# Kernel optimization log

Hardware: AMD Instinct MI355X
Metric: run time of the kernel (lower is better)

## Reference

```python
import jax, jax.numpy as jnp
import numpy as np

SEQ_LEN = 4096
N_FEATURES = 2048
N_HIDDEN = 2048
TAGS = 10
START_TAG = 8
STOP_TAG = 9
H = N_HIDDEN // 2  # per-direction hidden size


def setup_inputs() -> dict:
    key = jax.random.key(0)
    ks = jax.random.split(key, 10)
    s = 0.02
    sentence = jax.random.normal(ks[0], (SEQ_LEN, 1, N_FEATURES), jnp.float32)
    W_ih_f = jax.random.normal(ks[1], (4 * H, N_FEATURES), jnp.float32) * s
    W_hh_f = jax.random.normal(ks[2], (4 * H, H), jnp.float32) * s
    b_f = jax.random.normal(ks[3], (4 * H,), jnp.float32) * s
    W_ih_b = jax.random.normal(ks[4], (4 * H, N_FEATURES), jnp.float32) * s
    W_hh_b = jax.random.normal(ks[5], (4 * H, H), jnp.float32) * s
    b_b = jax.random.normal(ks[6], (4 * H,), jnp.float32) * s
    W_lin = jax.random.normal(ks[7], (TAGS, N_HIDDEN), jnp.float32) * s
    b_lin = jax.random.normal(ks[8], (TAGS,), jnp.float32) * s
    transitions = jax.random.normal(ks[9], (TAGS, TAGS), jnp.float32)
    transitions = transitions.at[START_TAG, :].set(-10000.0).at[:, STOP_TAG].set(-10000.0)
    return {"sentence": sentence, "W_ih_f": W_ih_f, "W_hh_f": W_hh_f, "b_f": b_f,
            "W_ih_b": W_ih_b, "W_hh_b": W_hh_b, "b_b": b_b,
            "W_lin": W_lin, "b_lin": b_lin, "transitions": transitions}


def _lstm_dir(x, W_ih, W_hh, b, reverse):
    # Precompute the input projection for all timesteps (one big GEMM).
    xp = jnp.einsum('tbf,gf->tbg', x, W_ih) + b  # [T, B, 4H]
    B = x.shape[1]
    init = (jnp.zeros((B, H), x.dtype), jnp.zeros((B, H), x.dtype))

    def step(carry, g):
        h, c = carry
        gates = g + h @ W_hh.T  # [B, 4H], PyTorch gate order i, f, g, o
        i, f, gg, o = jnp.split(gates, 4, axis=-1)
        c = jax.nn.sigmoid(f) * c + jax.nn.sigmoid(i) * jnp.tanh(gg)
        h = jax.nn.sigmoid(o) * jnp.tanh(c)
        return (h, c), h

    _, hs = jax.lax.scan(step, init, xp, reverse=reverse)
    return hs  # [T, B, H]


def reference(sentence, W_ih_f, W_hh_f, b_f, W_ih_b, W_hh_b, b_b, W_lin, b_lin, transitions):
    h_f = _lstm_dir(sentence, W_ih_f, W_hh_f, b_f, False)
    h_b = _lstm_dir(sentence, W_ih_b, W_hh_b, b_b, True)
    lstm_out = jnp.concatenate([h_f, h_b], axis=-1)         # [T, 1, N_HIDDEN]
    feats = lstm_out @ W_lin.T + b_lin                       # [T, 1, TAGS]
    f = feats[:, 0, :]                                       # [T, TAGS] (batch=1 as in original)

    init_v = jnp.full((TAGS,), -10000.0, f.dtype).at[START_TAG].set(0.0)

    def vstep(fv, feat):
        scores = fv[None, :] + transitions                   # [next_tag, prev_tag]
        return jnp.max(scores, axis=1) + feat, jnp.argmax(scores, axis=1)

    fv, bps = jax.lax.scan(vstep, init_v, f)                 # bps: [T, TAGS]
    terminal = fv + transitions[STOP_TAG]
    path_score = jnp.max(terminal)
    best_last = jnp.argmax(terminal)

    def bstep(tag, bp):
        return bp[tag], tag

    _, best_path = jax.lax.scan(bstep, best_last, bps, reverse=True)  # [T] in time order
    return path_score, best_path
```

## Files before the change

kernel.cpp:

```cpp
#include <hip/hip_runtime.h>

typedef _Float16 f16;
typedef _Float16 f16x4 __attribute__((ext_vector_type(4)));
typedef _Float16 f16x8 __attribute__((ext_vector_type(8)));
typedef float f32x4 __attribute__((ext_vector_type(4)));
typedef unsigned u32x4 __attribute__((ext_vector_type(4)));

#define SEQ 4096
#define NF  2048
#define HID 1024
#define SENT 0x7F800001u

__device__ f16   g_Ahi[SEQ * NF];
__device__ f16   g_Alo[SEQ * NF];
__device__ f16   g_Whi[2 * 4096 * NF];
__device__ f16   g_Wlo[2 * 4096 * NF];
__device__ float g_xp [2u * SEQ * 4096u];
__device__ float g_hist[2u * SEQ * HID];
__device__ float g_ring[2][8][1024];
__device__ float g_feats[SEQ * 10];

__global__ void cvt_split(const float* __restrict__ src, int which, int n4) {
  int i = blockIdx.x * blockDim.x + threadIdx.x;
  int stride = gridDim.x * blockDim.x;
  f16* hi; f16* lo;
  if (which == 0)      { hi = g_Ahi; lo = g_Alo; }
  else if (which == 1) { hi = g_Whi; lo = g_Wlo; }
  else                 { hi = g_Whi + 4096 * NF; lo = g_Wlo + 4096 * NF; }
  const float4* s4 = (const float4*)src;
  f16x4* h4 = (f16x4*)hi;
  f16x4* l4 = (f16x4*)lo;
  for (int idx = i; idx < n4; idx += stride) {
    float4 v = s4[idx];
    f16x4 h, l;
    h.x = (f16)v.x; l.x = (f16)(v.x - (float)h.x);
    h.y = (f16)v.y; l.y = (f16)(v.y - (float)h.y);
    h.z = (f16)v.z; l.z = (f16)(v.z - (float)h.z);
    h.w = (f16)v.w; l.w = (f16)(v.w - (float)h.w);
    h4[idx] = h; l4[idx] = l;
  }
}

__global__ __launch_bounds__(256, 1) void gemm_xp(
    const float* __restrict__ b_f, const float* __restrict__ b_b)
{
  const int d = blockIdx.z;
  const f16* WhiD = g_Whi + (size_t)d * (4096u * 2048u);
  const f16* WloD = g_Wlo + (size_t)d * (4096u * 2048u);
  const float* bias = d ? b_b : b_f;
  float* out = g_xp + (size_t)d * (4096u * 4096u);

  __shared__ f16 sAh[128 * 40];
  __shared__ f16 sAl[128 * 40];
  __shared__ f16 sWh[128 * 40];
  __shared__ f16 sWl[128 * 40];

  const int tid  = threadIdx.x;
  const int lane = tid & 63;
  const int wv   = tid >> 6;
  const int quad = lane >> 4;
  const int mrow = lane & 15;
  const int m0 = (wv & 1) * 64;
  const int n0 = (wv >> 1) * 64;
  const int bm = blockIdx.y, bn = blockIdx.x;

  f32x4 acc[4][4] = {};

  const int r0  = tid >> 2;
  const int seg = tid & 3;

  for (int kt = 0; kt < 2048; kt += 32) {
#pragma unroll
    for (int r = 0; r < 2; ++r) {
      int row = r * 64 + r0;
      size_t ga = (size_t)(bm * 128 + row) * 2048 + kt + seg * 8;
      size_t gw = (size_t)(bn * 128 + row) * 2048 + kt + seg * 8;
      int lidx = row * 40 + seg * 8;
      *(f16x8*)&sAh[lidx] = *(const f16x8*)&g_Ahi[ga];
      *(f16x8*)&sAl[lidx] = *(const f16x8*)&g_Alo[ga];
      *(f16x8*)&sWh[lidx] = *(const f16x8*)&WhiD[gw];
      *(f16x8*)&sWl[lidx] = *(const f16x8*)&WloD[gw];
    }
    __syncthreads();

    f16x8 ah[4], al[4], wh[4], wl[4];
#pragma unroll
    for (int mi = 0; mi < 4; ++mi) {
      int rowm = (m0 + mi * 16 + mrow) * 40 + quad * 8;
      ah[mi] = *(const f16x8*)&sAh[rowm];
      al[mi] = *(const f16x8*)&sAl[rowm];
    }
#pragma unroll
    for (int ni = 0; ni < 4; ++ni) {
      int rown = (n0 + ni * 16 + mrow) * 40 + quad * 8;
      wh[ni] = *(const f16x8*)&sWh[rown];
      wl[ni] = *(const f16x8*)&sWl[rown];
    }
#pragma unroll
    for (int mi = 0; mi < 4; ++mi)
#pragma unroll
      for (int ni = 0; ni < 4; ++ni) {
        acc[mi][ni] = __builtin_amdgcn_mfma_f32_16x16x32_f16(ah[mi], wh[ni], acc[mi][ni], 0, 0, 0);
        acc[mi][ni] = __builtin_amdgcn_mfma_f32_16x16x32_f16(ah[mi], wl[ni], acc[mi][ni], 0, 0, 0);
        acc[mi][ni] = __builtin_amdgcn_mfma_f32_16x16x32_f16(al[mi], wh[ni], acc[mi][ni], 0, 0, 0);
      }
    __syncthreads();
  }

#pragma unroll
  for (int ni = 0; ni < 4; ++ni) {
    int g = bn * 128 + n0 + ni * 16 + mrow;
    float bv = bias[g];
#pragma unroll
    for (int mi = 0; mi < 4; ++mi) {
#pragma unroll
      for (int r = 0; r < 4; ++r) {
        int t = bm * 128 + m0 + mi * 16 + quad * 4 + r;
        out[(size_t)t * 4096 + g] = acc[mi][ni][r] + bv;
      }
    }
  }
}

__global__ void init_sync() {
  int i = blockIdx.x * blockDim.x + threadIdx.x;
  int slot = (i >> 10) & 7;
  ((unsigned*)g_ring)[i] = (slot == 0) ? 0u : SENT;
}

__global__ __launch_bounds__(1024) void lstm_persistent(
    const float* __restrict__ Whh_f, const float* __restrict__ Whh_b)
{
  const int bid = blockIdx.x;
  const int dir = bid & 3;
  if (dir >= 2) return;
  const int wsl = bid >> 2;
  const int tid = threadIdx.x;
  const int r   = tid >> 4;
  const int l16 = tid & 15;

  __shared__ float h_lds[1024];
  __shared__ float gates_lds[64];

  const float* Wd = dir ? Whh_b : Whh_f;

  const int grow = (r >> 4) * 1024 + wsl * 16 + (r & 15);
  float4 w4[16];
#pragma unroll
  for (int j = 0; j < 16; ++j)
    w4[j] = *(const float4*)&Wd[(size_t)grow * 1024 + 4 * l16 + 64 * j];

  const float* xpd = g_xp + (size_t)dir * 4096u * 4096u;
  float* histd = g_hist + (size_t)dir * 4096u * 1024u;
  float* ringd = &g_ring[dir][0][0];

  float c = 0.f;

  for (int t = 1; t <= 4096; ++t) {
    const int tau = dir ? (4096 - t) : (t - 1);

    float xv0 = 0.f, xv1 = 0.f, xv2 = 0.f, xv3 = 0.f;
    if (tid < 16) {
      const float* px = xpd + (size_t)tau * 4096 + wsl * 16 + tid;
      xv0 = px[0]; xv1 = px[1024]; xv2 = px[2048]; xv3 = px[3072];
    }

    if (tid < 256) {
      const float* rs = ringd + (size_t)((t - 1) & 7) * 1024 + 4 * tid;
      u32x4 q;
      for (;;) {
        asm volatile("global_load_dwordx4 %0, %1, off sc0 sc1\n\t"
                     "s_waitcnt vmcnt(0)"
                     : "=v"(q) : "v"(rs) : "memory");
        if (q.x != SENT && q.y != SENT && q.z != SENT && q.w != SENT) break;
        __builtin_amdgcn_s_sleep(1);
      }
      float4 hv;
      hv.x = __uint_as_float(q.x);
      hv.y = __uint_as_float(q.y);
      hv.z = __uint_as_float(q.z);
      hv.w = __uint_as_float(q.w);
      *(float4*)&h_lds[4 * tid] = hv;
    }
    __syncthreads();

    float p0 = 0.f, p1 = 0.f, p2 = 0.f, p3 = 0.f;
#pragma unroll
    for (int j = 0; j < 16; j += 4) {
      float4 h0 = *(const float4*)&h_lds[4 * l16 + 64 * (j + 0)];
      float4 h1 = *(const float4*)&h_lds[4 * l16 + 64 * (j + 1)];
      float4 h2 = *(const float4*)&h_lds[4 * l16 + 64 * (j + 2)];
      float4 h3 = *(const float4*)&h_lds[4 * l16 + 64 * (j + 3)];
      p0 += w4[j+0].x*h0.x + w4[j+0].y*h0.y + w4[j+0].z*h0.z + w4[j+0].w*h0.w;
      p1 += w4[j+1].x*h1.x + w4[j+1].y*h1.y + w4[j+1].z*h1.z + w4[j+1].w*h1.w;
      p2 += w4[j+2].x*h2.x + w4[j+2].y*h2.y + w4[j+2].z*h2.z + w4[j+2].w*h2.w;
      p3 += w4[j+3].x*h3.x + w4[j+3].y*h3.y + w4[j+3].z*h3.z + w4[j+3].w*h3.w;
    }
    float acc = (p0 + p1) + (p2 + p3);
    acc += __shfl_xor(acc, 1);
    acc += __shfl_xor(acc, 2);
    acc += __shfl_xor(acc, 4);
    acc += __shfl_xor(acc, 8);
    if (l16 == 0) gates_lds[r] = acc;
    __syncthreads();

    if (tid < 16) {
      float gi = gates_lds[tid]      + xv0;
      float gf = gates_lds[16 + tid] + xv1;
      float gg = gates_lds[32 + tid] + xv2;
      float go = gates_lds[48 + tid] + xv3;
      float si = 1.f / (1.f + __expf(-gi));
      float sf = 1.f / (1.f + __expf(-gf));
      float so = 1.f / (1.f + __expf(-go));
      float tg = 1.f - 2.f / (1.f + __expf(2.f * gg));
      c = sf * c + si * tg;
      float th = 1.f - 2.f / (1.f + __expf(2.f * c));
      float h  = so * th;
      const int dim = wsl * 16 + tid;
      __hip_atomic_store((unsigned*)&ringd[(size_t)(t & 7) * 1024 + dim],
                         __float_as_uint(h),
                         __ATOMIC_RELAXED, __HIP_MEMORY_SCOPE_AGENT);
      if (t + 4 <= 4096)
        __hip_atomic_store((unsigned*)&ringd[(size_t)((t + 4) & 7) * 1024 + dim],
                           SENT,
                           __ATOMIC_RELAXED, __HIP_MEMORY_SCOPE_AGENT);
      histd[(size_t)tau * 1024 + dim] = h;
    }
  }
}

__global__ __launch_bounds__(256, 1) void feats_kernel(
    const float* __restrict__ W_lin, const float* __restrict__ b_lin)
{
  const int tid = threadIdx.x;
  const int wv = tid >> 6, l = tid & 63;
  const int t0 = blockIdx.x * 16 + wv * 4;
  for (int it = 0; it < 4; ++it) {
    const int t = t0 + it;
    float hf[16], hbv[16];
#pragma unroll
    for (int i = 0; i < 16; ++i) hf[i]  = g_hist[(size_t)t * 1024 + l + 64 * i];
#pragma unroll
    for (int i = 0; i < 16; ++i) hbv[i] = g_hist[(size_t)(4096 + t) * 1024 + l + 64 * i];
#pragma unroll
    for (int tag = 0; tag < 10; ++tag) {
      float a = 0.f;
#pragma unroll
      for (int i = 0; i < 16; ++i) {
        a += W_lin[tag * 2048 + l + 64 * i] * hf[i];
        a += W_lin[tag * 2048 + 1024 + l + 64 * i] * hbv[i];
      }
      a += __shfl_xor(a, 32); a += __shfl_xor(a, 16); a += __shfl_xor(a, 8);
      a += __shfl_xor(a, 4);  a += __shfl_xor(a, 2);  a += __shfl_xor(a, 1);
      if (l == 0) g_feats[t * 10 + tag] = a + b_lin[tag];
    }
  }
}

__global__ __launch_bounds__(64, 1) void viterbi_kernel(
    const float* __restrict__ trans, float* __restrict__ out)
{
  __shared__ unsigned char bps[4096 * 10];
  const int to = threadIdx.x;
  float tr[10];
#pragma unroll
  for (int f = 0; f < 10; ++f) tr[f] = (to < 10) ? trans[to * 10 + f] : 0.f;
  float fv = (to == 8) ? 0.f : -10000.f;

  float fbuf[8];
#pragma unroll
  for (int i = 0; i < 8; ++i) fbuf[i] = (to < 10) ? g_feats[i * 10 + to] : 0.f;

  for (int t = 0; t < 4096; t += 8) {
#pragma unroll
    for (int u = 0; u < 8; ++u) {
      const int tt = t + u;
      float m = -3.4e38f; int am = 0;
#pragma unroll
      for (int f = 0; f < 10; ++f) {
        float v = __shfl(fv, f) + tr[f];
        if (v > m) { m = v; am = f; }
      }
      float ft = fbuf[u];
      if (tt + 8 < 4096 && to < 10) fbuf[u] = g_feats[(tt + 8) * 10 + to];
      fv = m + ft;
      if (to < 10) bps[tt * 10 + to] = (unsigned char)am;
    }
  }
  __syncthreads();

  float term = fv + ((to < 10) ? trans[90 + to] : -3.4e38f);
  float best = -3.4e38f; int bl = 0;
#pragma unroll
  for (int f = 0; f < 10; ++f) {
    float v = __shfl(term, f);
    if (v > best) { best = v; bl = f; }
  }
  if (to == 0) {
    out[0] = best;
    int tag = bl;
    for (int t = 4095; t >= 0; --t) {
      out[1 + t] = (float)tag;
      tag = bps[t * 10 + tag];
    }
  }
}

extern "C" void kernel_launch(void* const* d_in, const int* in_sizes, int n_in,
                              void* d_out, int out_size, void* d_ws, size_t ws_size,
                              hipStream_t stream)
{
  (void)in_sizes; (void)n_in; (void)out_size; (void)d_ws; (void)ws_size;
  const float* W_hh_f   = (const float*)d_in[2];
  const float* b_f      = (const float*)d_in[3];
  const float* W_hh_b   = (const float*)d_in[5];
  const float* b_b      = (const float*)d_in[6];
  const float* W_lin    = (const float*)d_in[7];
  const float* b_lin    = (const float*)d_in[8];
  const float* trans    = (const float*)d_in[9];

  cvt_split<<<1024, 256, 0, stream>>>((const float*)d_in[0], 0, 2097152);
  cvt_split<<<1024, 256, 0, stream>>>((const float*)d_in[1], 1, 2097152);
  cvt_split<<<1024, 256, 0, stream>>>((const float*)d_in[4], 2, 2097152);

  gemm_xp<<<dim3(32, 32, 2), 256, 0, stream>>>(b_f, b_b);

  init_sync<<<16, 1024, 0, stream>>>();

  lstm_persistent<<<256, 1024, 0, stream>>>(W_hh_f, W_hh_b);

  feats_kernel<<<256, 256, 0, stream>>>(W_lin, b_lin);

  viterbi_kernel<<<1, 64, 0, stream>>>(trans, (float*)d_out);
}
```

Before: 10.68 ms.

## Map each wavefront to one hidden unit's four gates and drop second barrier

Reorganizes the persistent LSTM block so each wavefront owns all four gate rows of one hidden dimension, with each 16-lane group handling one gate. Gate pre-activations are gathered by wave shuffles and every lane computes the cell update, so the gates LDS array and the second __syncthreads per timestep go away. The h buffer in LDS is double-buffered so the next step's writes cannot race with reads that have not finished. Every thread now loads its own xp value, and the elementwise math is done redundantly across lanes.

```diff
diff --git a/kernel.cpp b/kernel.cpp
--- a/kernel.cpp
+++ b/kernel.cpp
@@ -135,16 +135,18 @@
   const int dir = bid & 3;
   if (dir >= 2) return;
   const int wsl = bid >> 2;
-  const int tid = threadIdx.x;
-  const int r   = tid >> 4;
-  const int l16 = tid & 15;
-
-  __shared__ float h_lds[1024];
-  __shared__ float gates_lds[64];
+  const int tid  = threadIdx.x;
+  const int w    = tid >> 6;
+  const int lane = tid & 63;
+  const int g    = lane >> 4;
+  const int l16  = lane & 15;
+
+  __shared__ float h_lds[2][1024];
 
   const float* Wd = dir ? Whh_b : Whh_f;
-
-  const int grow = (r >> 4) * 1024 + wsl * 16 + (r & 15);
+  const int dim  = wsl * 16 + w;
+  const int grow = g * 1024 + dim;
+
   float4 w4[16];
 #pragma unroll
   for (int j = 0; j < 16; ++j)
@@ -158,14 +160,9 @@
 
   for (int t = 1; t <= 4096; ++t) {
     const int tau = dir ? (4096 - t) : (t - 1);
-
-    float xv0 = 0.f, xv1 = 0.f, xv2 = 0.f, xv3 = 0.f;
-    if (tid < 16) {
-      const float* px = xpd + (size_t)tau * 4096 + wsl * 16 + tid;
-      xv0 = px[0]; xv1 = px[1024]; xv2 = px[2048]; xv3 = px[3072];
-    }
-
-    if (tid < 256) {
+    const int b   = (t - 1) & 1;
+
+    if (w < 4) {
       const float* rs = ringd + (size_t)((t - 1) & 7) * 1024 + 4 * tid;
       u32x4 q;
       for (;;) {
@@ -180,43 +177,41 @@
       hv.y = __uint_as_float(q.y);
       hv.z = __uint_as_float(q.z);
       hv.w = __uint_as_float(q.w);
-      *(float4*)&h_lds[4 * tid] = hv;
-    }
+      *(float4*)&h_lds[b][4 * tid] = hv;
+    }
+    float xv = xpd[(size_t)tau * 4096 + g * 1024 + dim];
     __syncthreads();
 
     float p0 = 0.f, p1 = 0.f, p2 = 0.f, p3 = 0.f;
 #pragma unroll
     for (int j = 0; j < 16; j += 4) {
-      float4 h0 = *(const float4*)&h_lds[4 * l16 + 64 * (j + 0)];
-      float4 h1 = *(const float4*)&h_lds[4 * l16 + 64 * (j + 1)];
-      float4 h2 = *(const float4*)&h_lds[4 * l16 + 64 * (j + 2)];
-      float4 h3 = *(const float4*)&h_lds[4 * l16 + 64 * (j + 3)];
+      float4 h0 = *(const float4*)&h_lds[b][4 * l16 + 64 * (j + 0)];
+      float4 h1 = *(const float4*)&h_lds[b][4 * l16 + 64 * (j + 1)];
+      float4 h2 = *(const float4*)&h_lds[b][4 * l16 + 64 * (j + 2)];
+      float4 h3 = *(const float4*)&h_lds[b][4 * l16 + 64 * (j + 3)];
       p0 += w4[j+0].x*h0.x + w4[j+0].y*h0.y + w4[j+0].z*h0.z + w4[j+0].w*h0.w;
       p1 += w4[j+1].x*h1.x + w4[j+1].y*h1.y + w4[j+1].z*h1.z + w4[j+1].w*h1.w;
       p2 += w4[j+2].x*h2.x + w4[j+2].y*h2.y + w4[j+2].z*h2.z + w4[j+2].w*h2.w;
       p3 += w4[j+3].x*h3.x + w4[j+3].y*h3.y + w4[j+3].z*h3.z + w4[j+3].w*h3.w;
     }
-    float acc = (p0 + p1) + (p2 + p3);
-    acc += __shfl_xor(acc, 1);
-    acc += __shfl_xor(acc, 2);
-    acc += __shfl_xor(acc, 4);
-    acc += __shfl_xor(acc, 8);
-    if (l16 == 0) gates_lds[r] = acc;
-    __syncthreads();
-
-    if (tid < 16) {
-      float gi = gates_lds[tid]      + xv0;
-      float gf = gates_lds[16 + tid] + xv1;
-      float gg = gates_lds[32 + tid] + xv2;
-      float go = gates_lds[48 + tid] + xv3;
-      float si = 1.f / (1.f + __expf(-gi));
-      float sf = 1.f / (1.f + __expf(-gf));
-      float so = 1.f / (1.f + __expf(-go));
-      float tg = 1.f - 2.f / (1.f + __expf(2.f * gg));
-      c = sf * c + si * tg;
-      float th = 1.f - 2.f / (1.f + __expf(2.f * c));
-      float h  = so * th;
-      const int dim = wsl * 16 + tid;
+    float val = (p0 + p1) + (p2 + p3);
+    val += __shfl_xor(val, 1);
+    val += __shfl_xor(val, 2);
+    val += __shfl_xor(val, 4);
+    val += __shfl_xor(val, 8);
+    val += xv;
+    float gi = __shfl(val, l16);
+    float gf = __shfl(val, l16 + 16);
+    float gg = __shfl(val, l16 + 32);
+    float go = __shfl(val, l16 + 48);
+    float si = 1.f / (1.f + __expf(-gi));
+    float sf = 1.f / (1.f + __expf(-gf));
+    float so = 1.f / (1.f + __expf(-go));
+    float tg = 1.f - 2.f / (1.f + __expf(2.f * gg));
+    c = sf * c + si * tg;
+    float th = 1.f - 2.f / (1.f + __expf(2.f * c));
+    float h  = so * th;
+    if (lane == 0) {
       __hip_atomic_store((unsigned*)&ringd[(size_t)(t & 7) * 1024 + dim],
                          __float_as_uint(h),
                          __ATOMIC_RELAXED, __HIP_MEMORY_SCOPE_AGENT);
```

Measured after the change: 23.43 ms. 2.19x slower.
